# Performance work log

Hardware: AMD Instinct MI355X
Metric: run time of the kernel (lower is better)

## Reference

```python
import jax, jax.numpy as jnp
import numpy as np

T, N, D, H = 512, 64, 1024, 1024  # time, batch(envs), input dim, hidden dim


def setup_inputs() -> dict:
    key = jax.random.key(0)
    ks = jax.random.split(key, 7)
    x = jax.random.normal(ks[0], (T, N, D), jnp.float32)
    hx = jax.random.normal(ks[1], (N, H), jnp.float32)
    mask = (jax.random.uniform(ks[2], (T, N)) > 0.05).astype(jnp.float32)
    s = float(1.0 / np.sqrt(H))
    w_ih = jax.random.uniform(ks[3], (3 * H, D), jnp.float32, -s, s)
    w_hh = jax.random.uniform(ks[4], (3 * H, H), jnp.float32, -s, s)
    b_ih = jax.random.uniform(ks[5], (3 * H,), jnp.float32, -s, s)
    b_hh = jax.random.uniform(ks[6], (3 * H,), jnp.float32, -s, s)
    return {"x": x, "hx": hx, "mask": mask, "w_ih": w_ih, "w_hh": w_hh,
            "b_ih": b_ih, "b_hh": b_hh}


def reference(x, hx, mask, w_ih, w_hh, b_ih, b_hh):
    """Masked GRU scan, equivalent to the segment-splitting torch loop:
    h is multiplied by mask[t] before every step (mask==1 inside episodes,
    0 at episode boundaries, so this matches masking only at segment starts).
    """
    # Precompute input projections for all timesteps in one big GEMM: [T,N,3H]
    gi = jnp.einsum('tnd,gd->tng', x, w_ih) + b_ih

    def step(h, inp):
        gi_t, m_t = inp                       # [N,3H], [N]
        h = h * m_t[:, None]                  # reset hidden at episode starts
        gh = h @ w_hh.T + b_hh                # [N,3H]
        i_r, i_z, i_n = jnp.split(gi_t, 3, axis=-1)
        h_r, h_z, h_n = jnp.split(gh, 3, axis=-1)
        r = jax.nn.sigmoid(i_r + h_r)
        z = jax.nn.sigmoid(i_z + h_z)
        n = jnp.tanh(i_n + r * h_n)
        h_new = (1.0 - z) * n + z * h
        return h_new, h_new

    h_final, out = jax.lax.scan(step, hx, (gi, mask))
    return out, h_final
```

## Files before the change

### kernel.cpp

```cpp
#include <hip/hip_runtime.h>

#define TT 512
#define NN 64
#define DD 1024
#define HH 1024
#define NSLOT 32

typedef __attribute__((ext_vector_type(8))) short bf16x8;
typedef __attribute__((ext_vector_type(4))) float f32x4;
typedef __attribute__((ext_vector_type(8))) unsigned short u16x8;
typedef __attribute__((ext_vector_type(4))) int i32x4;
typedef __attribute__((ext_vector_type(2))) int i32x2;

__device__ unsigned short g_wih[192u * 2048 * 8];
__device__ unsigned short g_whh[192u * 2048 * 8];
__device__ unsigned short g_x[2048u * 2048 * 8];
__device__ unsigned short g_gi[(size_t)2048 * 64 * 768];
__device__ unsigned g_hbuf32[(size_t)NSLOT * 4 * 16384];

__device__ __forceinline__ unsigned short f2bf(float f) {
  unsigned u = __float_as_uint(f);
  u += 0x7fffu + ((u >> 16) & 1u);
  return (unsigned short)(u >> 16);
}

__global__ void prep_kernel(const float* __restrict__ x,
                            const float* __restrict__ wih,
                            const float* __restrict__ whh) {
  const int gsz = gridDim.x * blockDim.x;
  const int gid = blockIdx.x * blockDim.x + threadIdx.x;
  for (int z = gid; z < NSLOT * 4 * 16384; z += gsz) g_hbuf32[z] = 0u;

  const int W8 = 192 * 2048;
  const int X8 = 2048 * 2048;
  for (int idx = gid; idx < 2 * W8 + X8; idx += gsz) {
    if (idx < 2 * W8) {
      const float* src = (idx < W8) ? wih : whh;
      unsigned short* dst = (idx < W8) ? g_wih : g_whh;
      int i8 = (idx < W8) ? idx : idx - W8;
      size_t g = (size_t)i8 * 8;
      int col = (int)(g >> 10);
      int k = (int)(g & 1023);
      int kk = k >> 5, lg = (k >> 3) & 3;
      int cg = col >> 4;
      int l = (col & 15) | (lg << 4);
      size_t o8 = ((size_t)cg * 32 + kk) * 64 + l;
      const float* p = src + g;
      float4 v0 = *(const float4*)(p);
      float4 v1 = *(const float4*)(p + 4);
      u16x8 u;
      u[0] = f2bf(v0.x); u[1] = f2bf(v0.y); u[2] = f2bf(v0.z); u[3] = f2bf(v0.w);
      u[4] = f2bf(v1.x); u[5] = f2bf(v1.y); u[6] = f2bf(v1.z); u[7] = f2bf(v1.w);
      *(u16x8*)(dst + o8 * 8) = u;
    } else {
      int i8 = idx - 2 * W8;
      size_t g = (size_t)i8 * 8;
      int row = (int)(g >> 10);
      int k = (int)(g & 1023);
      int t = row >> 6, env = row & 63;
      int eg = env >> 4;
      int kk = k >> 5, lg = (k >> 3) & 3;
      int l = (env & 15) | (lg << 4);
      size_t o8 = (((size_t)t * 4 + eg) * 32 + kk) * 64 + l;
      const float* p = x + g;
      float4 v0 = *(const float4*)(p);
      float4 v1 = *(const float4*)(p + 4);
      u16x8 u;
      u[0] = f2bf(v0.x); u[1] = f2bf(v0.y); u[2] = f2bf(v0.z); u[3] = f2bf(v0.w);
      u[4] = f2bf(v1.x); u[5] = f2bf(v1.y); u[6] = f2bf(v1.z); u[7] = f2bf(v1.w);
      *(u16x8*)(g_x + o8 * 8) = u;
    }
  }
}

__global__ __launch_bounds__(256) void gemm_gi() {
  extern __shared__ char smem[];
  unsigned short* As = (unsigned short*)smem;
  unsigned short* Bs = As + 2048 * 8;
  const int tid = threadIdx.x;
  const int bid = blockIdx.x;
  const int mblk = bid & 255, nblk = bid >> 8;
  const int w = tid >> 6, l = tid & 63;
  const int wm = w >> 1, wn = w & 1;

  u16x8 pa[8], pb[8];
  #pragma unroll
  for (int i = 0; i < 8; ++i) {
    int e = tid + i * 256;
    int mt = e >> 8, kkl = (e >> 6) & 3, lane = e & 63;
    pa[i] = *((const u16x8*)g_x  + ((size_t)(mblk * 8 + mt) * 32 + kkl) * 64 + lane);
    pb[i] = *((const u16x8*)g_wih + ((size_t)(nblk * 8 + mt) * 32 + kkl) * 64 + lane);
  }
  f32x4 acc[4][4] = {};
  for (int c = 0; c < 8; ++c) {
    __syncthreads();
    #pragma unroll
    for (int i = 0; i < 8; ++i) {
      int e = tid + i * 256;
      ((u16x8*)As)[e] = pa[i];
      ((u16x8*)Bs)[e] = pb[i];
    }
    __syncthreads();
    if (c < 7) {
      #pragma unroll
      for (int i = 0; i < 8; ++i) {
        int e = tid + i * 256;
        int mt = e >> 8, kkl = (e >> 6) & 3, lane = e & 63;
        pa[i] = *((const u16x8*)g_x  + ((size_t)(mblk * 8 + mt) * 32 + (c + 1) * 4 + kkl) * 64 + lane);
        pb[i] = *((const u16x8*)g_wih + ((size_t)(nblk * 8 + mt) * 32 + (c + 1) * 4 + kkl) * 64 + lane);
      }
    }
    #pragma unroll
    for (int kkl = 0; kkl < 4; ++kkl) {
      bf16x8 af[4], bfr[4];
      #pragma unroll
      for (int ai = 0; ai < 4; ++ai) af[ai]  = ((const bf16x8*)As)[((wm * 4 + ai) * 4 + kkl) * 64 + l];
      #pragma unroll
      for (int bi = 0; bi < 4; ++bi) bfr[bi] = ((const bf16x8*)Bs)[((wn * 4 + bi) * 4 + kkl) * 64 + l];
      #pragma unroll
      for (int ai = 0; ai < 4; ++ai)
        #pragma unroll
        for (int bi = 0; bi < 4; ++bi)
          acc[ai][bi] = __builtin_amdgcn_mfma_f32_16x16x32_bf16(af[ai], bfr[bi], acc[ai][bi], 0, 0, 0);
    }
  }
  const int jj = l & 15;
  #pragma unroll
  for (int ai = 0; ai < 4; ++ai)
    #pragma unroll
    for (int bi = 0; bi < 4; ++bi) {
      int mt = mblk * 8 + wm * 4 + ai;
      int nt = nblk * 8 + wn * 4 + bi;
      int gate = nt >> 6, jg = nt & 63;
      size_t base = ((size_t)mt * 64 + jg) * 768 + (size_t)gate * 256;
      #pragma unroll
      for (int i = 0; i < 4; ++i) {
        int env = (l >> 4) * 4 + i;
        g_gi[base + env * 16 + jj] = f2bf(acc[ai][bi][i]);
      }
    }
}

__global__ __launch_bounds__(256) void scan_kernel(const float* __restrict__ hx,
                                                   const float* __restrict__ mask,
                                                   const float* __restrict__ bih,
                                                   const float* __restrict__ bhh,
                                                   float* __restrict__ out) {
  extern __shared__ char smem[];
  unsigned short* whhL = (unsigned short*)smem;
  unsigned short* hA   = whhL + 3 * 2048 * 8;
  float* Cl = (float*)(hA + 2048 * 8);

  const int tid = threadIdx.x;
  const int bid = blockIdx.x;
  const int eg = bid >> 6, jg = bid & 63;
  const int e0 = eg * 16;
  const int w3 = tid >> 6, l = tid & 63;
  const int e_ = tid >> 4, jj = tid & 15;
  const int j = jg * 16 + jj;

  #pragma unroll 4
  for (int i = 0; i < 24; ++i) {
    int e = tid + i * 256;
    int gate = e >> 11, rem = e & 2047;
    ((u16x8*)whhL)[e] = *((const u16x8*)g_whh + (size_t)(gate * 64 + jg) * 2048 + rem);
  }

  const int kf = jg * 16 + jj;
  const int widx = (((kf >> 5) * 64) + (e_ | (((kf >> 3) & 3) << 4))) * 8 + (kf & 7);

  float hreg;
  {
    float h0 = hx[(size_t)(e0 + e_) * HH + j] * mask[e0 + e_];
    hreg = h0;
    unsigned tw = (1u << 16) | (unsigned)f2bf(h0);
    unsigned* dst = g_hbuf32 + ((size_t)eg << 14) + widx;
    asm volatile("global_store_dword %0, %1, off sc0 sc1" :: "v"(dst), "v"(tw) : "memory");
  }

  const float br  = bih[j] + bhh[j];
  const float bz  = bih[HH + j] + bhh[HH + j];
  const float bin = bih[2 * HH + j];
  const float bhn = bhh[2 * HH + j];

  unsigned short pgr0, pgz0, pgn0, pgr1, pgz1, pgn1;
  {
    size_t gb0 = ((size_t)eg * 64 + jg) * 768;
    pgr0 = g_gi[gb0 + tid]; pgz0 = g_gi[gb0 + 256 + tid]; pgn0 = g_gi[gb0 + 512 + tid];
    size_t gb1 = ((size_t)(4 + eg) * 64 + jg) * 768;
    pgr1 = g_gi[gb1 + tid]; pgz1 = g_gi[gb1 + 256 + tid]; pgn1 = g_gi[gb1 + 512 + tid];
  }

  const unsigned voff = (unsigned)tid * 16;

  for (int t = 0; t < TT; ++t) {
    int tm = (t + 1 < TT) ? (t + 1) : (TT - 1);
    float mnext = mask[tm * NN + e0 + e_];

    const unsigned* hb = g_hbuf32 + ((((size_t)(t & (NSLOT - 1))) * 4 + eg) << 14);
    const unsigned tagc = (unsigned)(t + 1);

    {
      const unsigned* pp = hb + (l << 8);
      while (true) {
        unsigned v;
        asm volatile("global_load_dword %0, %1, off sc0 sc1\n\t"
                     "s_waitcnt vmcnt(0)"
                     : "=v"(v) : "v"(pp) : "memory");
        if (__all((v >> 16) >= tagc)) break;
        __builtin_amdgcn_s_sleep(1);
      }
      __builtin_amdgcn_sched_barrier(0);
    }

    const unsigned tagp = tagc << 16;
    const i32x4* hp = (const i32x4*)hb + tid;
    i32x4 hv[16];
    #pragma unroll
    for (int c = 0; c < 16; ++c) hv[c] = hp[c * 256];

    unsigned stale = 0;
    #pragma unroll
    for (int c = 0; c < 16; ++c) {
      unsigned bad = (((unsigned)hv[c][0] ^ tagp) | ((unsigned)hv[c][1] ^ tagp) |
                      ((unsigned)hv[c][2] ^ tagp) | ((unsigned)hv[c][3] ^ tagp)) & 0xFFFF0000u;
      if (bad) stale |= (1u << c);
      else {
        i32x2 pk;
        pk[0] = (int)__builtin_amdgcn_perm((unsigned)hv[c][1], (unsigned)hv[c][0], 0x05040100u);
        pk[1] = (int)__builtin_amdgcn_perm((unsigned)hv[c][3], (unsigned)hv[c][2], 0x05040100u);
        ((i32x2*)hA)[c * 256 + tid] = pk;
      }
    }
    while (__any(stale != 0)) {
      #pragma unroll
      for (int c = 0; c < 16; ++c) if (stale & (1u << c)) {
        asm volatile("global_load_dwordx4 %0, %1, %2 sc0 sc1"
                     : "=v"(hv[c]) : "v"(voff), "s"((const void*)(hb + c * 1024)));
      }
      asm volatile("s_waitcnt vmcnt(0)" ::: "memory");
      __builtin_amdgcn_sched_barrier(0);
      #pragma unroll
      for (int c = 0; c < 16; ++c) if (stale & (1u << c)) {
        unsigned bad = (((unsigned)hv[c][0] ^ tagp) | ((unsigned)hv[c][1] ^ tagp) |
                        ((unsigned)hv[c][2] ^ tagp) | ((unsigned)hv[c][3] ^ tagp)) & 0xFFFF0000u;
        if (!bad) {
          i32x2 pk;
          pk[0] = (int)__builtin_amdgcn_perm((unsigned)hv[c][1], (unsigned)hv[c][0], 0x05040100u);
          pk[1] = (int)__builtin_amdgcn_perm((unsigned)hv[c][3], (unsigned)hv[c][2], 0x05040100u);
          ((i32x2*)hA)[c * 256 + tid] = pk;
          stale &= ~(1u << c);
        }
      }
    }
    __syncthreads();

    float gr  = __uint_as_float((unsigned)pgr0 << 16);
    float gz  = __uint_as_float((unsigned)pgz0 << 16);
    float gn_ = __uint_as_float((unsigned)pgn0 << 16);
    pgr0 = pgr1; pgz0 = pgz1; pgn0 = pgn1;
    {
      int t2 = (t + 2 < TT) ? (t + 2) : (TT - 1);
      size_t gb = ((size_t)(t2 * 4 + eg) * 64 + jg) * 768;
      pgr1 = g_gi[gb + tid]; pgz1 = g_gi[gb + 256 + tid]; pgn1 = g_gi[gb + 512 + tid];
    }

    if (w3 < 3) {
      const bf16x8* ap = (const bf16x8*)hA;
      const bf16x8* bp = (const bf16x8*)whhL + (size_t)w3 * 2048;
      f32x4 a0 = {0.f,0.f,0.f,0.f}, a1 = {0.f,0.f,0.f,0.f};
      f32x4 a2 = {0.f,0.f,0.f,0.f}, a3 = {0.f,0.f,0.f,0.f};
      #pragma unroll 8
      for (int kk = 0; kk < 8; ++kk) {
        a0 = __builtin_amdgcn_mfma_f32_16x16x32_bf16(ap[kk * 64 + l],        bp[kk * 64 + l],        a0, 0, 0, 0);
        a1 = __builtin_amdgcn_mfma_f32_16x16x32_bf16(ap[(kk + 8) * 64 + l],  bp[(kk + 8) * 64 + l],  a1, 0, 0, 0);
        a2 = __builtin_amdgcn_mfma_f32_16x16x32_bf16(ap[(kk + 16) * 64 + l], bp[(kk + 16) * 64 + l], a2, 0, 0, 0);
        a3 = __builtin_amdgcn_mfma_f32_16x16x32_bf16(ap[(kk + 24) * 64 + l], bp[(kk + 24) * 64 + l], a3, 0, 0, 0);
      }
      f32x4 s;
      #pragma unroll
      for (int i = 0; i < 4; ++i) s[i] = (a0[i] + a1[i]) + (a2[i] + a3[i]);
      int col = l & 15, r0 = (l >> 4) * 4;
      #pragma unroll
      for (int i = 0; i < 4; ++i) Cl[w3 * 256 + (r0 + i) * 16 + col] = s[i];
    }
    __syncthreads();

    {
      float pr = gr + Cl[tid] + br;
      float pz = gz + Cl[256 + tid] + bz;
      float r = 1.f / (1.f + __expf(-pr));
      float z = 1.f / (1.f + __expf(-pz));
      float hn = Cl[512 + tid] + bhn;
      float gn = gn_ + bin + r * hn;
      float e2g = __expf(2.f * gn);
      float n = 1.f - 2.f / (e2g + 1.f);
      float hnew = (1.f - z) * n + z * hreg;

      if (t + 1 < TT) {
        float hm = hnew * mnext;
        hreg = hm;
        unsigned tw = ((unsigned)(t + 2) << 16) | (unsigned)f2bf(hm);
        unsigned* dst = g_hbuf32 + ((((size_t)((t + 1) & (NSLOT - 1))) * 4 + eg) << 14) + widx;
        asm volatile("global_store_dword %0, %1, off sc0 sc1" :: "v"(dst), "v"(tw) : "memory");
      }

      out[(size_t)t * NN * HH + (size_t)(e0 + e_) * HH + j] = hnew;
      if (t == TT - 1)
        out[(size_t)TT * NN * HH + (size_t)(e0 + e_) * HH + j] = hnew;
    }
  }
}

extern "C" void kernel_launch(void* const* d_in, const int* in_sizes, int n_in,
                              void* d_out, int out_size, void* d_ws, size_t ws_size,
                              hipStream_t stream) {
  (void)in_sizes; (void)n_in; (void)d_ws; (void)ws_size; (void)out_size;
  const float* x    = (const float*)d_in[0];
  const float* hx   = (const float*)d_in[1];
  const float* mask = (const float*)d_in[2];
  const float* wih  = (const float*)d_in[3];
  const float* whh  = (const float*)d_in[4];
  const float* bih  = (const float*)d_in[5];
  const float* bhh  = (const float*)d_in[6];
  float* out = (float*)d_out;

  hipFuncSetAttribute((const void*)gemm_gi, hipFuncAttributeMaxDynamicSharedMemorySize, 65536);
  hipFuncSetAttribute((const void*)scan_kernel, hipFuncAttributeMaxDynamicSharedMemorySize, 134144);

  prep_kernel<<<2048, 256, 0, stream>>>(x, wih, whh);
  gemm_gi<<<6144, 256, 65536, stream>>>();
  scan_kernel<<<256, 256, 134144, stream>>>(hx, mask, bih, bhh, out);
}
```

Baseline: 1.976 ms.

## Replace per-element tag polling with per-wave signal flags for cross-block sync

Adds a compact signal array in which each wave publishes its step tag after its hidden-state stores drain. One wave per block polls 256 flags with dwordx4 loads and releases the other waves through a shared-memory flag. The aim is to cut polling traffic on the big hidden buffer. The cost is an extra s_waitcnt on every store, an extra global store per wave, and intra-block spinning on LDS.

```diff
diff --git a/kernel.cpp b/kernel.cpp
--- a/kernel.cpp
+++ b/kernel.cpp
@@ -17,6 +17,7 @@
 __device__ unsigned short g_x[2048u * 2048 * 8];
 __device__ unsigned short g_gi[(size_t)2048 * 64 * 768];
 __device__ unsigned g_hbuf32[(size_t)NSLOT * 4 * 16384];
+__device__ int g_sig[NSLOT * 4 * 256];
 
 __device__ __forceinline__ unsigned short f2bf(float f) {
   unsigned u = __float_as_uint(f);
@@ -30,6 +31,7 @@
   const int gsz = gridDim.x * blockDim.x;
   const int gid = blockIdx.x * blockDim.x + threadIdx.x;
   for (int z = gid; z < NSLOT * 4 * 16384; z += gsz) g_hbuf32[z] = 0u;
+  for (int z = gid; z < NSLOT * 4 * 256; z += gsz) g_sig[z] = 0;
 
   const int W8 = 192 * 2048;
   const int X8 = 2048 * 2048;
@@ -150,6 +152,7 @@
   unsigned short* whhL = (unsigned short*)smem;
   unsigned short* hA   = whhL + 3 * 2048 * 8;
   float* Cl = (float*)(hA + 2048 * 8);
+  __shared__ int sFlag;
 
   const int tid = threadIdx.x;
   const int bid = blockIdx.x;
@@ -177,6 +180,14 @@
     unsigned* dst = g_hbuf32 + ((size_t)eg << 14) + widx;
     asm volatile("global_store_dword %0, %1, off sc0 sc1" :: "v"(dst), "v"(tw) : "memory");
   }
+  asm volatile("s_waitcnt vmcnt(0)" ::: "memory");
+  if (l == 0) {
+    int* sp0 = g_sig + (eg << 8) + (jg << 2) + w3;
+    int one = 1;
+    asm volatile("global_store_dword %0, %1, off sc0 sc1" :: "v"(sp0), "v"(one) : "memory");
+  }
+  if (tid == 0) sFlag = 0;
+  __syncthreads();
 
   const float br  = bih[j] + bhh[j];
   const float bz  = bih[HH + j] + bhh[HH + j];
@@ -197,21 +208,27 @@
     int tm = (t + 1 < TT) ? (t + 1) : (TT - 1);
     float mnext = mask[tm * NN + e0 + e_];
 
-    const unsigned* hb = g_hbuf32 + ((((size_t)(t & (NSLOT - 1))) * 4 + eg) << 14);
+    const int slot = t & (NSLOT - 1);
+    const unsigned* hb = g_hbuf32 + (((size_t)slot * 4 + eg) << 14);
     const unsigned tagc = (unsigned)(t + 1);
 
-    {
-      const unsigned* pp = hb + (l << 8);
+    if (w3 == 0) {
+      const int* sp = g_sig + ((slot * 4 + eg) << 8) + (l << 2);
       while (true) {
-        unsigned v;
-        asm volatile("global_load_dword %0, %1, off sc0 sc1\n\t"
+        i32x4 sv;
+        asm volatile("global_load_dwordx4 %0, %1, off sc0 sc1\n\t"
                      "s_waitcnt vmcnt(0)"
-                     : "=v"(v) : "v"(pp) : "memory");
-        if (__all((v >> 16) >= tagc)) break;
+                     : "=v"(sv) : "v"(sp) : "memory");
+        int mn = min(min(sv[0], sv[1]), min(sv[2], sv[3]));
+        if (__all(mn >= (int)tagc)) break;
         __builtin_amdgcn_s_sleep(1);
       }
-      __builtin_amdgcn_sched_barrier(0);
-    }
+      if (tid == 0) *((volatile int*)&sFlag) = (int)tagc;
+    } else {
+      volatile int* vf = &sFlag;
+      while (*vf < (int)tagc) __builtin_amdgcn_s_sleep(1);
+    }
+    __builtin_amdgcn_sched_barrier(0);
 
     const unsigned tagp = tagc << 16;
     const i32x4* hp = (const i32x4*)hb + tid;
@@ -303,6 +320,12 @@
         unsigned tw = ((unsigned)(t + 2) << 16) | (unsigned)f2bf(hm);
         unsigned* dst = g_hbuf32 + ((((size_t)((t + 1) & (NSLOT - 1))) * 4 + eg) << 14) + widx;
         asm volatile("global_store_dword %0, %1, off sc0 sc1" :: "v"(dst), "v"(tw) : "memory");
+        asm volatile("s_waitcnt vmcnt(0)" ::: "memory");
+        if (l == 0) {
+          int* sp = g_sig + ((((t + 1) & (NSLOT - 1)) * 4 + eg) << 8) + (jg << 2) + w3;
+          int tv = t + 2;
+          asm volatile("global_store_dword %0, %1, off sc0 sc1" :: "v"(sp), "v"(tv) : "memory");
+        }
       }
 
       out[(size_t)t * NN * HH + (size_t)(e0 + e_) * HH + j] = hnew;
```

New measurement: 5.466 ms. +176.6%, slower.
